# Kernel optimization log

Measured on AMD Instinct MI355X. Metric: run time of the kernel, lower is better.

The kernel has to match this reference:

```python
import jax, jax.numpy as jnp
import numpy as np

B, T, U, V = 8, 128, 64, 512
BLANK = 0
NEG_INF = -1e30  # finite 'log zero' to keep gradients NaN-free


def setup_inputs() -> dict:
    key = jax.random.key(0)
    k1, k2, k3, k4, k5 = jax.random.split(key, 5)
    emissions = jax.random.normal(k1, (B, T, V), dtype=jnp.float32)
    predictions = jax.random.normal(k2, (B, U, V), dtype=jnp.float32)
    labels = jax.random.randint(k3, (B, U - 1), 1, V, dtype=jnp.int32)
    # max(input_lengths) must equal T; max(label_lengths) must equal U-1
    input_lengths = jax.random.randint(k4, (B,), T // 2, T + 1, dtype=jnp.int32).at[0].set(T)
    label_lengths = jax.random.randint(k5, (B,), (U - 1) // 2, U, dtype=jnp.int32).at[0].set(U - 1)
    return {
        "emissions": emissions,
        "predictions": predictions,
        "labels": labels,
        "input_lengths": input_lengths,
        "label_lengths": label_lengths,
    }


def _rnnt_costs(emissions, predictions, labels, input_lengths, label_lengths, blank=BLANK):
    b, t_len, v = emissions.shape
    u_len = predictions.shape[1]
    # joint lattice log-probs: log_softmax over vocab of additive joint
    log_probs = jax.nn.log_softmax(
        emissions[:, :, None, :] + predictions[:, None, :, :], axis=-1
    )  # (B, T, U, V)
    blank_lp = log_probs[..., blank]  # (B, T, U)
    lbl = jnp.broadcast_to(labels[:, None, :, None], (b, t_len, u_len - 1, 1))
    label_lp = jnp.take_along_axis(log_probs[:, :, : u_len - 1, :], lbl, axis=3)[..., 0]  # (B,T,U-1)

    def step(a_top, xs):
        # a_top[b,u] = alpha[t-1,u] + blank_lp[t-1,u]  (entry-from-above scores)
        blank_t, label_t = xs  # (B,U), (B,U-1)
        # c[u] = sum_{k<u} label_lp[t,k]  -> alpha[t,u] = c[u] + LSE_{u'<=u}(a_top[u'] - c[u'])
        c = jnp.concatenate(
            [jnp.zeros((b, 1), a_top.dtype), jnp.cumsum(label_t, axis=1)], axis=1
        )  # (B, U)
        alpha_t = c + jax.lax.cumlogsumexp(a_top - c, axis=1)
        a_next = alpha_t + blank_t  # alpha[t,u] + blank_lp[t,u]
        return a_next, a_next

    a0 = jnp.full((b, u_len), NEG_INF, dtype=emissions.dtype).at[:, 0].set(0.0)
    xs = (jnp.moveaxis(blank_lp, 1, 0), jnp.moveaxis(label_lp, 1, 0))
    _, scores = jax.lax.scan(step, a0, xs)  # (T, B, U): alpha[t,u]+blank_lp[t,u]
    scores = jnp.moveaxis(scores, 1, 0)  # (B, T, U)
    bidx = jnp.arange(b)
    # cost_b = -(alpha[T_b-1, U_b] + blank_lp[T_b-1, U_b])
    costs = -scores[bidx, input_lengths - 1, label_lengths]
    return costs


def reference(emissions, predictions, labels, input_lengths, label_lengths):
    return _rnnt_costs(emissions, predictions, labels, input_lengths, label_lengths)
```

## Files before the change

### kernel.cpp

```cpp
#include <hip/hip_runtime.h>

#define B 8
#define T 128
#define U 64
#define V 512
#define ROWS (T + 2)
#define PADK 520
#define LN2 0.6931471805599453f

typedef __attribute__((ext_vector_type(8))) short bf8v;
typedef __attribute__((ext_vector_type(4))) float f4v;

template<int CTRL, int ROWM>
__device__ __forceinline__ float dpp_movf(float x, int old_bits) {
    int r = __builtin_amdgcn_update_dpp(old_bits, __builtin_bit_cast(int, x),
                                        CTRL, ROWM, 0xF, false);
    return __builtin_bit_cast(float, r);
}
__device__ __forceinline__ float wave_max63(float x) {
    const int NI = (int)0xff800000u;
    x = fmaxf(x, dpp_movf<0x111, 0xF>(x, NI));
    x = fmaxf(x, dpp_movf<0x112, 0xF>(x, NI));
    x = fmaxf(x, dpp_movf<0x114, 0xF>(x, NI));
    x = fmaxf(x, dpp_movf<0x118, 0xF>(x, NI));
    x = fmaxf(x, dpp_movf<0x142, 0xA>(x, NI));
    x = fmaxf(x, dpp_movf<0x143, 0xC>(x, NI));
    return x;
}
__device__ __forceinline__ float rdlane(float x, int lane) {
    return __builtin_bit_cast(float,
        __builtin_amdgcn_readlane(__builtin_bit_cast(int, x), lane));
}
__device__ __forceinline__ float dpp_shr1(float x) {
    int r = __builtin_amdgcn_update_dpp(0, __builtin_bit_cast(int, x),
                                        0x138, 0xF, 0xF, false);
    return __builtin_bit_cast(float, r);
}

__device__ __forceinline__ short f2bf(float x) {
    unsigned b = __builtin_bit_cast(unsigned, x);
    unsigned r = (b + 0x7FFFu + ((b >> 16) & 1u)) >> 16;
    return (short)r;
}
__device__ __forceinline__ float bf2f(short h) {
    return __builtin_bit_cast(float, ((unsigned)(unsigned short)h) << 16);
}

__global__ __launch_bounds__(1024) void fused_kernel(
    const float* __restrict__ em, const float* __restrict__ pr,
    const int* __restrict__ labels,
    const int* __restrict__ in_len, const int* __restrict__ lab_len,
    float* __restrict__ out)
{
    __shared__ __align__(16) char smemRaw[2 * 64 * PADK * 2];
    __shared__ float Pp0s[U], Ppls[U], Ee0s[T];
    __shared__ int   lbls[U];

    short*  Ph = (short*)smemRaw;
    short*  Pl = Ph + 64 * PADK;
    float2* QI = (float2*)smemRaw;

    const int b    = blockIdx.x;
    const int tid  = threadIdx.x;
    const int lane = tid & 63;
    const int w    = tid >> 6;

    if (tid < T)     Ee0s[tid] = __expf(em[((size_t)b * T + tid) * V]);
    if (tid < U)     Pp0s[tid] = __expf(pr[((size_t)b * U + tid) * V]);
    if (tid < U - 1) {
        const int lb = labels[b * (U - 1) + tid];
        lbls[tid] = lb;
        Ppls[tid] = __expf(pr[((size_t)b * U + tid) * V + lb]);
    }

    for (int idx = tid; idx < 64 * 64; idx += 1024) {
        const int u = idx >> 6, c = idx & 63;
        const float* prow = pr + ((size_t)b * U + u) * V + c * 8;
        const float4 f0 = ((const float4*)prow)[0];
        const float4 f1 = ((const float4*)prow)[1];
        const float e[8] = {f0.x, f0.y, f0.z, f0.w, f1.x, f1.y, f1.z, f1.w};
        bf8v hi, lo;
        #pragma unroll
        for (int j = 0; j < 8; ++j) {
            const float x = __expf(e[j]);
            const short h = f2bf(x);
            hi[j] = h;
            lo[j] = f2bf(x - bf2f(h));
        }
        ((bf8v*)Ph)[u * (PADK / 8) + c] = hi;
        ((bf8v*)Pl)[u * (PADK / 8) + c] = lo;
    }
    __syncthreads();

    f4v acc[2];
    acc[0] = (f4v){0.f, 0.f, 0.f, 0.f};
    acc[1] = (f4v){0.f, 0.f, 0.f, 0.f};

    const int arow = lane & 15;
    const int kb   = (lane >> 4) * 8;
    const int mt   = w >> 1;
    const int nb   = (w & 1) * 2;

    {
        const int t = mt * 16 + arow;
        const float* erow = em + ((size_t)b * T + t) * V;
        #pragma unroll 2
        for (int ks = 0; ks < 16; ++ks) {
            const int k0 = ks * 32 + kb;
            const float4 f0 = ((const float4*)(erow + k0))[0];
            const float4 f1 = ((const float4*)(erow + k0))[1];
            const float e[8] = {f0.x, f0.y, f0.z, f0.w, f1.x, f1.y, f1.z, f1.w};
            bf8v ah, al;
            #pragma unroll
            for (int j = 0; j < 8; ++j) {
                const float x = __expf(e[j]);
                const short h = f2bf(x);
                ah[j] = h;
                al[j] = f2bf(x - bf2f(h));
            }
            #pragma unroll
            for (int j = 0; j < 2; ++j) {
                const int bu = (nb + j) * 16 + arow;
                const bf8v bh = ((const bf8v*)Ph)[bu * (PADK / 8) + k0 / 8];
                const bf8v bl = ((const bf8v*)Pl)[bu * (PADK / 8) + k0 / 8];
                acc[j] = __builtin_amdgcn_mfma_f32_16x16x32_bf16(ah, bh, acc[j], 0, 0, 0);
                acc[j] = __builtin_amdgcn_mfma_f32_16x16x32_bf16(ah, bl, acc[j], 0, 0, 0);
                acc[j] = __builtin_amdgcn_mfma_f32_16x16x32_bf16(al, bh, acc[j], 0, 0, 0);
            }
        }
    }
    __syncthreads();

    for (int i = tid; i < ROWS * U; i += 1024) QI[i] = make_float2(0.f, 0.f);
    __syncthreads();

    const int ccol  = lane & 15;
    const int crow0 = (lane >> 4) * 4;
    #pragma unroll
    for (int j = 0; j < 2; ++j) {
        const int u = (nb + j) * 16 + ccol;
        #pragma unroll
        for (int r = 0; r < 4; ++r) {
            const int t = mt * 16 + crow0 + r;
            const float inv = 1.0f / acc[j][r];
            QI[(t + 1) * U + u].x = Ee0s[t] * Pp0s[u] * inv;
            if (u < U - 1) {
                const float eel = __expf(em[((size_t)b * T + t) * V + lbls[u]]);
                QI[t * U + (u + 1)].y = eel * Ppls[u] * inv;
            }
        }
    }
    __syncthreads();
    if (tid >= 64) return;

    const int u  = tid;
    const int Tb = in_len[b];
    const int Ub = lab_len[b];
    const int dmax = (Tb - 1) + Ub;

    auto qidx = [&](int d) {
        int r = d - u;
        r = min(max(r, 0), T + 1);
        return r * U + u;
    };

    float A = (u == 0) ? 1.0f : 0.0f;
    int   off = 0;
    float aCap = 1.0f;
    int   offCap = 0;
    float sPend = 1.0f;
    int   ePend = 0;

    float2 c8[8], n8[8];
    #pragma unroll
    for (int j = 0; j < 8; ++j) c8[j] = QI[qidx(1 + j)];

    for (int d0 = 1; d0 <= 185; d0 += 8) {
        #pragma unroll
        for (int j = 0; j < 8; ++j) {
            n8[j] = QI[qidx(d0 + 8 + j)];
            A = fmaf(A, c8[j].x, dpp_shr1(A) * c8[j].y);
            if ((j & 3) == 3) {
                A *= sPend;
                off += ePend;
                const float mx = rdlane(wave_max63(A), 63);
                int e = ((__builtin_bit_cast(int, mx) >> 23) & 255) - 127;
                e = max(e, -96);
                sPend = __builtin_bit_cast(float, (157 - e) << 23);
                ePend = e - 30;
            }
            const bool cap = (d0 + j == dmax);
            aCap   = cap ? A   : aCap;
            offCap = cap ? off : offCap;
        }
        #pragma unroll
        for (int j = 0; j < 8; ++j) c8[j] = n8[j];
    }

    if (u == Ub) {
        const float bprob = QI[Tb * U + u].x;
        out[b] = -(__log2f(aCap) + (float)offCap + __log2f(bprob)) * LN2;
    }
}

extern "C" void kernel_launch(void* const* d_in, const int* in_sizes, int n_in,
                              void* d_out, int out_size, void* d_ws, size_t ws_size,
                              hipStream_t stream) {
    const float* em      = (const float*)d_in[0];
    const float* pr      = (const float*)d_in[1];
    const int*   labels  = (const int*)d_in[2];
    const int*   in_len  = (const int*)d_in[3];
    const int*   lab_len = (const int*)d_in[4];
    float* out = (float*)d_out;

    fused_kernel<<<B, 1024, 0, stream>>>(em, pr, labels, in_len, lab_len, out);
}
```

Baseline: 34.35 us.

## Split fused kernel into parallel joint-prob kernel and per-batch alpha recursion kernel

```diff
diff --git a/kernel.cpp b/kernel.cpp
--- a/kernel.cpp
+++ b/kernel.cpp
@@ -46,35 +46,42 @@
     return __builtin_bit_cast(float, ((unsigned)(unsigned short)h) << 16);
 }
 
-__global__ __launch_bounds__(1024) void fused_kernel(
+__global__ __launch_bounds__(512) void lp_kernel(
     const float* __restrict__ em, const float* __restrict__ pr,
     const int* __restrict__ labels,
-    const int* __restrict__ in_len, const int* __restrict__ lab_len,
-    float* __restrict__ out)
+    float* __restrict__ blankP, float* __restrict__ labelP)
 {
-    __shared__ __align__(16) char smemRaw[2 * 64 * PADK * 2];
-    __shared__ float Pp0s[U], Ppls[U], Ee0s[T];
-    __shared__ int   lbls[U];
-
-    short*  Ph = (short*)smemRaw;
-    short*  Pl = Ph + 64 * PADK;
-    float2* QI = (float2*)smemRaw;
-
-    const int b    = blockIdx.x;
+    __shared__ __align__(16) short Ph[32 * PADK];
+    __shared__ __align__(16) short Pl[32 * PADK];
+    __shared__ float Ee0s[64], Pp0s[32], Ppls[32];
+    __shared__ int   lbls[32];
+
+    const int bid  = blockIdx.x;
+    const int uh   = bid & 1;
+    const int th   = (bid >> 1) & 1;
+    const int b    = bid >> 2;
     const int tid  = threadIdx.x;
     const int lane = tid & 63;
     const int w    = tid >> 6;
 
-    if (tid < T)     Ee0s[tid] = __expf(em[((size_t)b * T + tid) * V]);
-    if (tid < U)     Pp0s[tid] = __expf(pr[((size_t)b * U + tid) * V]);
-    if (tid < U - 1) {
-        const int lb = labels[b * (U - 1) + tid];
-        lbls[tid] = lb;
-        Ppls[tid] = __expf(pr[((size_t)b * U + tid) * V + lb]);
-    }
-
-    for (int idx = tid; idx < 64 * 64; idx += 1024) {
-        const int u = idx >> 6, c = idx & 63;
+    if (tid < 64)
+        Ee0s[tid] = __expf(em[((size_t)b * T + th * 64 + tid) * V]);
+    if (tid < 32) {
+        const int u = uh * 32 + tid;
+        Pp0s[tid] = __expf(pr[((size_t)b * U + u) * V]);
+        if (u < U - 1) {
+            const int lb = labels[b * (U - 1) + u];
+            lbls[tid] = lb;
+            Ppls[tid] = __expf(pr[((size_t)b * U + u) * V + lb]);
+        } else {
+            lbls[tid] = 0;
+            Ppls[tid] = 0.0f;
+        }
+    }
+
+    for (int idx = tid; idx < 32 * 64; idx += 512) {
+        const int ul = idx >> 6, c = idx & 63;
+        const int u  = uh * 32 + ul;
         const float* prow = pr + ((size_t)b * U + u) * V + c * 8;
         const float4 f0 = ((const float4*)prow)[0];
         const float4 f1 = ((const float4*)prow)[1];
@@ -87,68 +94,77 @@
             hi[j] = h;
             lo[j] = f2bf(x - bf2f(h));
         }
-        ((bf8v*)Ph)[u * (PADK / 8) + c] = hi;
-        ((bf8v*)Pl)[u * (PADK / 8) + c] = lo;
+        ((bf8v*)Ph)[ul * (PADK / 8) + c] = hi;
+        ((bf8v*)Pl)[ul * (PADK / 8) + c] = lo;
     }
     __syncthreads();
 
-    f4v acc[2];
-    acc[0] = (f4v){0.f, 0.f, 0.f, 0.f};
-    acc[1] = (f4v){0.f, 0.f, 0.f, 0.f};
-
+    const int mt   = w >> 1;
+    const int ntl  = w & 1;
     const int arow = lane & 15;
     const int kb   = (lane >> 4) * 8;
-    const int mt   = w >> 1;
-    const int nb   = (w & 1) * 2;
-
-    {
-        const int t = mt * 16 + arow;
-        const float* erow = em + ((size_t)b * T + t) * V;
-        #pragma unroll 2
-        for (int ks = 0; ks < 16; ++ks) {
-            const int k0 = ks * 32 + kb;
-            const float4 f0 = ((const float4*)(erow + k0))[0];
-            const float4 f1 = ((const float4*)(erow + k0))[1];
-            const float e[8] = {f0.x, f0.y, f0.z, f0.w, f1.x, f1.y, f1.z, f1.w};
-            bf8v ah, al;
-            #pragma unroll
-            for (int j = 0; j < 8; ++j) {
-                const float x = __expf(e[j]);
-                const short h = f2bf(x);
-                ah[j] = h;
-                al[j] = f2bf(x - bf2f(h));
-            }
-            #pragma unroll
-            for (int j = 0; j < 2; ++j) {
-                const int bu = (nb + j) * 16 + arow;
-                const bf8v bh = ((const bf8v*)Ph)[bu * (PADK / 8) + k0 / 8];
-                const bf8v bl = ((const bf8v*)Pl)[bu * (PADK / 8) + k0 / 8];
-                acc[j] = __builtin_amdgcn_mfma_f32_16x16x32_bf16(ah, bh, acc[j], 0, 0, 0);
-                acc[j] = __builtin_amdgcn_mfma_f32_16x16x32_bf16(ah, bl, acc[j], 0, 0, 0);
-                acc[j] = __builtin_amdgcn_mfma_f32_16x16x32_bf16(al, bh, acc[j], 0, 0, 0);
-            }
-        }
-    }
-    __syncthreads();
-
-    for (int i = tid; i < ROWS * U; i += 1024) QI[i] = make_float2(0.f, 0.f);
-    __syncthreads();
+
+    f4v acc = (f4v){0.f, 0.f, 0.f, 0.f};
+    const int t_load = th * 64 + mt * 16 + arow;
+    const float* erow = em + ((size_t)b * T + t_load) * V;
+    const int bu = ntl * 16 + arow;
+
+    #pragma unroll 4
+    for (int ks = 0; ks < 16; ++ks) {
+        const int k0 = ks * 32 + kb;
+        const float4 f0 = ((const float4*)(erow + k0))[0];
+        const float4 f1 = ((const float4*)(erow + k0))[1];
+        const float e[8] = {f0.x, f0.y, f0.z, f0.w, f1.x, f1.y, f1.z, f1.w};
+        bf8v ah, al;
+        #pragma unroll
+        for (int j = 0; j < 8; ++j) {
+            const float x = __expf(e[j]);
+            const short h = f2bf(x);
+            ah[j] = h;
+            al[j] = f2bf(x - bf2f(h));
+        }
+        const bf8v bh = ((const bf8v*)Ph)[bu * (PADK / 8) + k0 / 8];
+        const bf8v bl = ((const bf8v*)Pl)[bu * (PADK / 8) + k0 / 8];
+        acc = __builtin_amdgcn_mfma_f32_16x16x32_bf16(ah, bh, acc, 0, 0, 0);
+        acc = __builtin_amdgcn_mfma_f32_16x16x32_bf16(ah, bl, acc, 0, 0, 0);
+        acc = __builtin_amdgcn_mfma_f32_16x16x32_bf16(al, bh, acc, 0, 0, 0);
+    }
 
     const int ccol  = lane & 15;
     const int crow0 = (lane >> 4) * 4;
+    const int ul    = ntl * 16 + ccol;
+    const int u     = uh * 32 + ul;
     #pragma unroll
-    for (int j = 0; j < 2; ++j) {
-        const int u = (nb + j) * 16 + ccol;
-        #pragma unroll
-        for (int r = 0; r < 4; ++r) {
-            const int t = mt * 16 + crow0 + r;
-            const float inv = 1.0f / acc[j][r];
-            QI[(t + 1) * U + u].x = Ee0s[t] * Pp0s[u] * inv;
-            if (u < U - 1) {
-                const float eel = __expf(em[((size_t)b * T + t) * V + lbls[u]]);
-                QI[t * U + (u + 1)].y = eel * Ppls[u] * inv;
-            }
-        }
+    for (int r = 0; r < 4; ++r) {
+        const int tl = mt * 16 + crow0 + r;
+        const int t  = th * 64 + tl;
+        const float inv = 1.0f / acc[r];
+        const size_t o = ((size_t)b * T + t) * U + u;
+        blankP[o] = Ee0s[tl] * Pp0s[ul] * inv;
+        if (u < U - 1) {
+            const float eel = __expf(em[((size_t)b * T + t) * V + lbls[ul]]);
+            labelP[o] = eel * Ppls[ul] * inv;
+        }
+    }
+}
+
+__global__ __launch_bounds__(256) void alpha_kernel(
+    const float* __restrict__ blankP, const float* __restrict__ labelP,
+    const int* __restrict__ in_len, const int* __restrict__ lab_len,
+    float* __restrict__ out)
+{
+    __shared__ float2 QI[ROWS * U];
+
+    const int b   = blockIdx.x;
+    const int tid = threadIdx.x;
+
+    const float* gb = blankP + (size_t)b * T * U;
+    const float* gl = labelP + (size_t)b * T * U;
+    for (int i = tid; i < ROWS * U; i += 256) {
+        const int r = i >> 6, u = i & 63;
+        const float x = (r >= 1 && r <= T) ? gb[(r - 1) * U + u] : 0.0f;
+        const float y = (r <= T - 1 && u >= 1) ? gl[r * U + u - 1] : 0.0f;
+        QI[i] = make_float2(x, y);
     }
     __syncthreads();
     if (tid >= 64) return;
@@ -213,5 +229,9 @@
     const int*   lab_len = (const int*)d_in[4];
     float* out = (float*)d_out;
 
-    fused_kernel<<<B, 1024, 0, stream>>>(em, pr, labels, in_len, lab_len, out);
-}
+    float* blankP = (float*)d_ws;
+    float* labelP = blankP + (size_t)B * T * U;
+
+    lp_kernel<<<B * 4, 512, 0, stream>>>(em, pr, labels, blankP, labelP);
+    alpha_kernel<<<B, 256, 0, stream>>>(blankP, labelP, in_len, lab_len, out);
+}
```

Measured after the change: 36.38 us. +5.9%, slower.
